# Optimization experiments

Measured on AMD Instinct MI355X. Metric: run time of the kernel, lower is better.

## Reference

```python
import jax, jax.numpy as jnp
import numpy as np

B, M, N, Z = 4, 64, 64, 64
IN_DIM, OUT_DIM = 32, 32
MODES1 = MODES2 = MODES3 = 16
HIDDEN = OUT_DIM * 4  # factor=4, n_ff_layers=2
LN_EPS = 1e-5


def setup_inputs() -> dict:
    key = jax.random.key(0)
    ks = jax.random.split(key, 10)
    # xavier-normal-ish scale for (in, out, modes, 2) fourier weights
    fscale = np.sqrt(2.0 / (IN_DIM + OUT_DIM))
    x = jax.random.normal(ks[0], (B, M, N, Z, IN_DIM), dtype=jnp.float32)
    wx = jax.random.normal(ks[1], (IN_DIM, OUT_DIM, MODES1, 2), dtype=jnp.float32) * fscale
    wy = jax.random.normal(ks[2], (IN_DIM, OUT_DIM, MODES2, 2), dtype=jnp.float32) * fscale
    wz = jax.random.normal(ks[3], (IN_DIM, OUT_DIM, MODES3, 2), dtype=jnp.float32) * fscale
    # FeedForward: Linear(OUT_DIM, HIDDEN) + ReLU, then Linear(HIDDEN, OUT_DIM) + LayerNorm
    w0 = jax.random.normal(ks[4], (OUT_DIM, HIDDEN), dtype=jnp.float32) * np.sqrt(1.0 / OUT_DIM)
    b0 = jnp.zeros((HIDDEN,), dtype=jnp.float32)
    w1 = jax.random.normal(ks[5], (HIDDEN, OUT_DIM), dtype=jnp.float32) * np.sqrt(1.0 / HIDDEN)
    b1 = jnp.zeros((OUT_DIM,), dtype=jnp.float32)
    ln_g = jnp.ones((OUT_DIM,), dtype=jnp.float32)
    ln_b = jnp.zeros((OUT_DIM,), dtype=jnp.float32)
    return {"x": x, "wx": wx, "wy": wy, "wz": wz,
            "w0": w0, "b0": b0, "w1": w1, "b1": b1,
            "ln_g": ln_g, "ln_b": ln_b}


def _as_complex(w):
    return w[..., 0] + 1j * w[..., 1]


def _forward_fourier(x, wx, wy, wz):
    # x: [b, m, n, z, i] -> [b, i, m, n, z]
    xt = jnp.transpose(x, (0, 4, 1, 2, 3))
    # --- axis M (dim 2) ---
    ftx = jnp.fft.rfft(xt, axis=2, norm='ortho')  # [b, i, M//2+1, n, z] complex
    ox = jnp.einsum('bixyz,iox->boxyz', ftx[:, :, :MODES1], _as_complex(wx))
    ox = jnp.pad(ox, ((0, 0), (0, 0), (0, M // 2 + 1 - MODES1), (0, 0), (0, 0)))
    xx = jnp.fft.irfft(ox, n=M, axis=2, norm='ortho')
    # --- axis N (dim 3) ---
    fty = jnp.fft.rfft(xt, axis=3, norm='ortho')
    oy = jnp.einsum('bixyz,ioy->boxyz', fty[:, :, :, :MODES2], _as_complex(wy))
    oy = jnp.pad(oy, ((0, 0), (0, 0), (0, 0), (0, N // 2 + 1 - MODES2), (0, 0)))
    xy = jnp.fft.irfft(oy, n=N, axis=3, norm='ortho')
    # --- axis Z (dim 4) ---
    ftz = jnp.fft.rfft(xt, axis=4, norm='ortho')
    oz = jnp.einsum('bixyz,ioz->boxyz', ftz[:, :, :, :, :MODES3], _as_complex(wz))
    oz = jnp.pad(oz, ((0, 0), (0, 0), (0, 0), (0, 0), (0, Z // 2 + 1 - MODES3)))
    xz = jnp.fft.irfft(oz, n=Z, axis=4, norm='ortho')
    out = xx + xy + xz  # [b, o, m, n, z]
    return jnp.transpose(out, (0, 2, 3, 4, 1))  # [b, m, n, z, o]


def reference(x, wx, wy, wz, w0, b0, w1, b1, ln_g, ln_b):
    s = _forward_fourier(x, wx, wy, wz)
    h = jax.nn.relu(s @ w0 + b0)
    y = h @ w1 + b1
    mu = jnp.mean(y, axis=-1, keepdims=True)
    var = jnp.mean((y - mu) ** 2, axis=-1, keepdims=True)
    y = (y - mu) * jax.lax.rsqrt(var + LN_EPS) * ln_g + ln_b
    return y
```

## Files before the change

### kernel.cpp

```cpp
#include <hip/hip_runtime.h>
#include <math.h>

typedef __attribute__((ext_vector_type(8))) short short8v;
typedef __attribute__((ext_vector_type(4))) float float4v;

constexpr float THETA = 6.28318530717958647692f / 64.0f;

constexpr int S_B = 64 * 64 * 64 * 32;
constexpr int S_M = 64 * 64 * 32;
constexpr int S_N = 64 * 32;
constexpr int S_Z = 32;

__device__ __forceinline__ unsigned short f2bf(float f) {
    unsigned int u = __builtin_bit_cast(unsigned int, f);
    u += 0x7FFFu + ((u >> 16) & 1u);
    return (unsigned short)(u >> 16);
}

constexpr int WS_TF = 98304, WS_TI = 100352, WS_TOTAL = 102400;

__global__ __launch_bounds__(256)
void setup_frags(const float* __restrict__ wx, const float* __restrict__ wy,
                 const float* __restrict__ wz, unsigned short* __restrict__ W)
{
    int f0 = (blockIdx.x * 256 + threadIdx.x) * 4;
#pragma unroll
    for (int u = 0; u < 4; ++u) {
        int f = f0 + u;
        unsigned short v;
        if (f < WS_TF) {
            int ax = f >> 15, rem = f & 32767;
            int k = rem >> 11;
            int rem2 = rem & 2047;
            int wt = rem2 >> 10, rt = (rem2 >> 9) & 1, l = (rem2 >> 3) & 63, e = rem2 & 7;
            int o = 16 * rt + (l & 15), i = 8 * (l >> 4) + e;
            const float* w = (ax == 0) ? wx : ((ax == 1) ? wy : wz);
            v = f2bf(w[((i * 32 + o) * 16 + k) * 2 + wt]);
        } else if (f < WS_TI) {
            int rem = f - WS_TF;
            int jt = rem >> 10, s = (rem >> 9) & 1, l = (rem >> 3) & 63, e = rem & 7;
            int kk = l & 15, m = 32 * s + 8 * (l >> 4) + e;
            int jm = (kk * m) & 63;
            float ang = THETA * (float)jm;
            v = f2bf(jt == 0 ? cosf(ang) : sinf(ang));
        } else {
            int rem = f - WS_TI;
            int mt = rem >> 9, l = (rem >> 3) & 63, e = rem & 7;
            int mp = 16 * mt + (l & 15), r = 8 * (l >> 4) + e;
            int k = r & 15;
            float sk = (k == 0) ? (1.0f / 64.0f) : (2.0f / 64.0f);
            int jm = (k * mp) & 63;
            float ang = THETA * (float)jm;
            v = f2bf(r < 16 ? sk * cosf(ang) : -sk * sinf(ang));
        }
        W[f] = v;
    }
}

__device__ __forceinline__ int ab_byte(int t, int k, int line, int i) {
    return ((((t * 16 + k) * 16 + line) * 64) + i * 2) ^ (((line ^ k) & 7) << 4);
}
__device__ __forceinline__ int p7i(int o, int line, int r) {
    return (o * 16 + line) * 40 + r;
}

template <int AXIS, bool ACCUM>
__global__ __launch_bounds__(256)
void spectral_mfma(const float* __restrict__ x,
                   const unsigned short* __restrict__ wf,
                   const unsigned short* __restrict__ tf,
                   const unsigned short* __restrict__ ti,
                   float* __restrict__ out)
{
    __shared__ __align__(16) unsigned short AB[16384];
    __shared__ __align__(16) unsigned short P7[20480];

    const int t = threadIdx.x, lane = t & 63, wave = t >> 6;
    const int gq = lane >> 4, c = lane & 15;
    constexpr int stride = (AXIS == 0) ? S_M : ((AXIS == 1) ? S_N : S_Z);
    const int l0 = blockIdx.x * 16;

    short8v tfB[2][2];
#pragma unroll
    for (int jt = 0; jt < 2; ++jt)
#pragma unroll
        for (int s = 0; s < 2; ++s)
            tfB[jt][s] = *reinterpret_cast<const short8v*>(tf + ((jt * 2 + s) * 64 + lane) * 8);

    for (int li = 0; li < 4; ++li) {
        const int line = wave * 4 + li;
        const int l = l0 + line;
        const int b = l >> 12, p1 = (l >> 6) & 63, p2 = l & 63;
        long bs;
        if (AXIS == 0)      bs = (long)b * S_B + (long)p1 * S_N + (long)p2 * S_Z;
        else if (AXIS == 1) bs = (long)b * S_B + (long)p1 * S_M + (long)p2 * S_Z;
        else                bs = (long)b * S_B + (long)p1 * S_M + (long)p2 * S_N;

        float4v acc[2][2];
#pragma unroll
        for (int rt = 0; rt < 2; ++rt)
#pragma unroll
            for (int jt = 0; jt < 2; ++jt)
                acc[rt][jt] = float4v{0.f, 0.f, 0.f, 0.f};

#pragma unroll
        for (int rt = 0; rt < 2; ++rt) {
            const float* xp = x + bs + 16 * rt + c;
#pragma unroll
            for (int s = 0; s < 2; ++s) {
                short8v a;
#pragma unroll
                for (int e = 0; e < 8; ++e)
                    a[e] = (short)f2bf(xp[(long)(32 * s + 8 * gq + e) * stride]);
                acc[rt][0] = __builtin_amdgcn_mfma_f32_16x16x32_bf16(a, tfB[0][s], acc[rt][0], 0, 0, 0);
                acc[rt][1] = __builtin_amdgcn_mfma_f32_16x16x32_bf16(a, tfB[1][s], acc[rt][1], 0, 0, 0);
            }
        }
#pragma unroll
        for (int rt = 0; rt < 2; ++rt)
#pragma unroll
            for (int jt = 0; jt < 2; ++jt) {
                unsigned int lo = (unsigned int)f2bf(acc[rt][jt][0]) | ((unsigned int)f2bf(acc[rt][jt][1]) << 16);
                unsigned int hi = (unsigned int)f2bf(acc[rt][jt][2]) | ((unsigned int)f2bf(acc[rt][jt][3]) << 16);
                *reinterpret_cast<uint2*>(reinterpret_cast<char*>(AB) + ab_byte(jt, c, line, 16 * rt + 4 * gq)) =
                    make_uint2(lo, hi);
            }
    }
    __syncthreads();

    {
        const int t2 = wave >> 1, rt = wave & 1;
        for (int k = 0; k < 16; k += 2) {
            float4v acc2[2];
#pragma unroll
            for (int kk = 0; kk < 2; ++kk) {
                const int kc = k + kk;
                short8v aT = *reinterpret_cast<const short8v*>(reinterpret_cast<const char*>(AB) + ab_byte(0, kc, c, 8 * gq));
                short8v bT = *reinterpret_cast<const short8v*>(reinterpret_cast<const char*>(AB) + ab_byte(1, kc, c, 8 * gq));
                const int w1t = t2 ? 1 : 0, w2t = t2 ? 0 : 1;
                short8v w1 = *reinterpret_cast<const short8v*>(wf + (((kc * 2 + w1t) * 2 + rt) * 64 + lane) * 8);
                short8v w2 = *reinterpret_cast<const short8v*>(wf + (((kc * 2 + w2t) * 2 + rt) * 64 + lane) * 8);
                if (t2) {
                    union { short8v s; unsigned int u[4]; } nb;
                    nb.s = bT;
#pragma unroll
                    for (int j = 0; j < 4; ++j) nb.u[j] ^= 0x80008000u;
                    bT = nb.s;
                }
                float4v a2 = float4v{0.f, 0.f, 0.f, 0.f};
                a2 = __builtin_amdgcn_mfma_f32_16x16x32_bf16(w1, aT, a2, 0, 0, 0);
                a2 = __builtin_amdgcn_mfma_f32_16x16x32_bf16(w2, bT, a2, 0, 0, 0);
                acc2[kk] = a2;
            }
#pragma unroll
            for (int r = 0; r < 4; ++r) {
                unsigned int u = (unsigned int)f2bf(acc2[0][r]) | ((unsigned int)f2bf(acc2[1][r]) << 16);
                *reinterpret_cast<unsigned int*>(&P7[p7i(16 * rt + 4 * gq + r, c, 16 * t2 + k)]) = u;
            }
        }
    }
    __syncthreads();

    short8v tiB[4];
#pragma unroll
    for (int mt = 0; mt < 4; ++mt)
        tiB[mt] = *reinterpret_cast<const short8v*>(ti + (mt * 64 + lane) * 8);

    for (int li = 0; li < 4; ++li) {
        const int line = wave * 4 + li;
        const int l = l0 + line;
        const int b = l >> 12, p1 = (l >> 6) & 63, p2 = l & 63;
        long bs;
        if (AXIS == 0)      bs = (long)b * S_B + (long)p1 * S_N + (long)p2 * S_Z;
        else if (AXIS == 1) bs = (long)b * S_B + (long)p1 * S_M + (long)p2 * S_Z;
        else                bs = (long)b * S_B + (long)p1 * S_M + (long)p2 * S_N;

        short8v pA[2];
        pA[0] = *reinterpret_cast<const short8v*>(&P7[p7i(c,      line, 8 * gq)]);
        pA[1] = *reinterpret_cast<const short8v*>(&P7[p7i(16 + c, line, 8 * gq)]);

#pragma unroll
        for (int rt = 0; rt < 2; ++rt)
#pragma unroll
            for (int mt = 0; mt < 4; ++mt) {
                float4v acc = float4v{0.f, 0.f, 0.f, 0.f};
                acc = __builtin_amdgcn_mfma_f32_16x16x32_bf16(pA[rt], tiB[mt], acc, 0, 0, 0);
                float* op = out + bs + (long)(16 * mt + c) * stride + 16 * rt + 4 * gq;
                if (ACCUM) {
                    float4 old = *reinterpret_cast<const float4*>(op);
                    old.x += acc[0]; old.y += acc[1]; old.z += acc[2]; old.w += acc[3];
                    *reinterpret_cast<float4*>(op) = old;
                } else {
                    *reinterpret_cast<float4*>(op) = make_float4(acc[0], acc[1], acc[2], acc[3]);
                }
            }
    }
}

__global__ __launch_bounds__(256)
void ffn_ln_mfma_kernel(float* __restrict__ io,
                        const float* __restrict__ w0, const float* __restrict__ b0,
                        const float* __restrict__ w1, const float* __restrict__ b1,
                        const float* __restrict__ g,  const float* __restrict__ bb)
{
    __shared__ unsigned short smem[28672];

    const int t = threadIdx.x;
    const int lane = t & 63, wave = t >> 6;
    const int gq = lane >> 4, c = lane & 15;

    for (int s = t; s < 512; s += 256) {
        const int n = s >> 6, ln = s & 63, g2 = ln >> 4, c2 = ln & 15;
        const int kb = n >> 1, nn = n & 1;
        short8v v0, v1;
#pragma unroll
        for (int e = 0; e < 8; ++e) {
            v0[e] = (short)f2bf(w0[(8 * g2 + e) * 128 + n * 16 + c2]);
            v1[e] = (short)f2bf(w1[(32 * kb + 8 * g2 + e) * 32 + nn * 16 + c2]);
        }
        *reinterpret_cast<short8v*>(&smem[s * 8])        = v0;
        *reinterpret_cast<short8v*>(&smem[4096 + s * 8]) = v1;
    }
    __syncthreads();

    float b0v[8], b1v[2], gv[2], bv[2];
#pragma unroll
    for (int n = 0; n < 8; ++n) b0v[n] = b0[n * 16 + c];
#pragma unroll
    for (int n = 0; n < 2; ++n) { b1v[n] = b1[n * 16 + c]; gv[n] = g[n * 16 + c]; bv[n] = bb[n * 16 + c]; }

    const int Hbase = 8192 + wave * 5120;

    for (int ti = 0; ti < 4; ++ti) {
        const int tile = (blockIdx.x * 4 + wave) * 4 + ti;
        const long p0 = (long)tile * 64;
        float* pio = io + p0 * 32;

        short8v af[4];
#pragma unroll
        for (int f = 0; f < 4; ++f) {
            const float* sp = pio + (16 * f + c) * 32 + 8 * gq;
            float4 lo = *reinterpret_cast<const float4*>(sp);
            float4 hi = *reinterpret_cast<const float4*>(sp + 4);
            af[f][0] = (short)f2bf(lo.x); af[f][1] = (short)f2bf(lo.y);
            af[f][2] = (short)f2bf(lo.z); af[f][3] = (short)f2bf(lo.w);
            af[f][4] = (short)f2bf(hi.x); af[f][5] = (short)f2bf(hi.y);
            af[f][6] = (short)f2bf(hi.z); af[f][7] = (short)f2bf(hi.w);
        }

        float4v Y[4][2];
#pragma unroll
        for (int f = 0; f < 4; ++f)
#pragma unroll
            for (int n = 0; n < 2; ++n)
                Y[f][n] = float4v{b1v[n], b1v[n], b1v[n], b1v[n]};

#pragma unroll
        for (int kb = 0; kb < 4; ++kb) {
            const int rb = (kb & 1) * 64;
#pragma unroll
            for (int nn = 0; nn < 2; ++nn) {
                const int n = 2 * kb + nn;
                const short8v wv = *reinterpret_cast<const short8v*>(&smem[(n * 64 + lane) * 8]);
#pragma unroll
                for (int f = 0; f < 4; ++f) {
                    float4v hacc = float4v{b0v[n], b0v[n], b0v[n], b0v[n]};
                    hacc = __builtin_amdgcn_mfma_f32_16x16x32_bf16(af[f], wv, hacc, 0, 0, 0);
#pragma unroll
                    for (int r = 0; r < 4; ++r) {
                        const float hv = fmaxf(hacc[r], 0.0f);
                        smem[Hbase + (rb + 16 * f + 4 * gq + r) * 40 + nn * 16 + c] = f2bf(hv);
                    }
                }
            }
            const short8v wva = *reinterpret_cast<const short8v*>(&smem[4096 + ((kb * 2 + 0) * 64 + lane) * 8]);
            const short8v wvb = *reinterpret_cast<const short8v*>(&smem[4096 + ((kb * 2 + 1) * 64 + lane) * 8]);
#pragma unroll
            for (int f = 0; f < 4; ++f) {
                const short8v a2 = *reinterpret_cast<const short8v*>(&smem[Hbase + (rb + 16 * f + c) * 40 + 8 * gq]);
                Y[f][0] = __builtin_amdgcn_mfma_f32_16x16x32_bf16(a2, wva, Y[f][0], 0, 0, 0);
                Y[f][1] = __builtin_amdgcn_mfma_f32_16x16x32_bf16(a2, wvb, Y[f][1], 0, 0, 0);
            }
        }

#pragma unroll
        for (int f = 0; f < 4; ++f) {
            float sm[4], sq[4];
#pragma unroll
            for (int r = 0; r < 4; ++r) {
                const float v0 = Y[f][0][r], v1 = Y[f][1][r];
                sm[r] = v0 + v1;
                sq[r] = v0 * v0 + v1 * v1;
            }
#pragma unroll
            for (int mask = 1; mask <= 8; mask <<= 1) {
#pragma unroll
                for (int r = 0; r < 4; ++r) {
                    sm[r] += __shfl_xor(sm[r], mask);
                    sq[r] += __shfl_xor(sq[r], mask);
                }
            }
#pragma unroll
            for (int r = 0; r < 4; ++r) {
                const float mu = sm[r] * (1.0f / 32.0f);
                const float var = sq[r] * (1.0f / 32.0f) - mu * mu;
                const float rs = rsqrtf(var + 1e-5f);
                float* op = io + (p0 + 16 * f + 4 * gq + r) * 32;
                op[c]      = (Y[f][0][r] - mu) * rs * gv[0] + bv[0];
                op[16 + c] = (Y[f][1][r] - mu) * rs * gv[1] + bv[1];
            }
        }
    }
}

extern "C" void kernel_launch(void* const* d_in, const int* in_sizes, int n_in,
                              void* d_out, int out_size, void* d_ws, size_t ws_size,
                              hipStream_t stream)
{
    const float* x    = (const float*)d_in[0];
    const float* wx   = (const float*)d_in[1];
    const float* wy   = (const float*)d_in[2];
    const float* wz   = (const float*)d_in[3];
    const float* w0   = (const float*)d_in[4];
    const float* b0   = (const float*)d_in[5];
    const float* w1   = (const float*)d_in[6];
    const float* b1   = (const float*)d_in[7];
    const float* ln_g = (const float*)d_in[8];
    const float* ln_b = (const float*)d_in[9];
    float* out = (float*)d_out;

    unsigned short* wsf = (unsigned short*)d_ws;

    setup_frags<<<100, 256, 0, stream>>>(wx, wy, wz, wsf);

    spectral_mfma<0, false><<<1024, 256, 0, stream>>>(x, wsf + 0 * 32768, wsf + WS_TF, wsf + WS_TI, out);
    spectral_mfma<1, true ><<<1024, 256, 0, stream>>>(x, wsf + 1 * 32768, wsf + WS_TF, wsf + WS_TI, out);
    spectral_mfma<2, true ><<<1024, 256, 0, stream>>>(x, wsf + 2 * 32768, wsf + WS_TF, wsf + WS_TI, out);

    ffn_ln_mfma_kernel<<<1024, 256, 0, stream>>>(out, w0, b0, w1, b1, ln_g, ln_b);
}
```

Measured before the change: 273.6 us.

## Fuse Z-axis spectral pass with FFN and LayerNorm, halve lines per block

```diff
diff --git a/kernel.cpp b/kernel.cpp
--- a/kernel.cpp
+++ b/kernel.cpp
@@ -27,6 +27,7 @@
 #pragma unroll
     for (int u = 0; u < 4; ++u) {
         int f = f0 + u;
+        if (f >= WS_TOTAL) continue;
         unsigned short v;
         if (f < WS_TF) {
             int ax = f >> 15, rem = f & 32767;
@@ -57,11 +58,103 @@
     }
 }
 
-__device__ __forceinline__ int ab_byte(int t, int k, int line, int i) {
-    return ((((t * 16 + k) * 16 + line) * 64) + i * 2) ^ (((line ^ k) & 7) << 4);
-}
-__device__ __forceinline__ int p7i(int o, int line, int r) {
-    return (o * 16 + line) * 40 + r;
+constexpr int AB_SHORTS = 8192;
+__device__ __forceinline__ int ab8(int t, int k, int line, int i) {
+    return ((((t * 16 + k) * 8 + line) * 64) + i * 2) ^ (((line ^ k) & 7) << 4);
+}
+constexpr int P_LS = 1288;
+constexpr int P_SHORTS = 8 * P_LS;
+__device__ __forceinline__ int p8(int line, int o, int r) {
+    return line * P_LS + o * 40 + r;
+}
+
+template <int STRIDE>
+__device__ __forceinline__ void stageF(const float* __restrict__ x,
+                                       const long* base2,
+                                       const unsigned short* __restrict__ tf,
+                                       unsigned short* __restrict__ AB,
+                                       int lane, int wave)
+{
+    const int gq = lane >> 4, c = lane & 15;
+    short8v tfB[2][2];
+#pragma unroll
+    for (int jt = 0; jt < 2; ++jt)
+#pragma unroll
+        for (int s = 0; s < 2; ++s)
+            tfB[jt][s] = *reinterpret_cast<const short8v*>(tf + ((jt * 2 + s) * 64 + lane) * 8);
+
+#pragma unroll
+    for (int li = 0; li < 2; ++li) {
+        const int line = wave * 2 + li;
+        float4v acc[2][2];
+#pragma unroll
+        for (int rt = 0; rt < 2; ++rt)
+#pragma unroll
+            for (int jt = 0; jt < 2; ++jt)
+                acc[rt][jt] = float4v{0.f, 0.f, 0.f, 0.f};
+
+#pragma unroll
+        for (int rt = 0; rt < 2; ++rt) {
+            const float* xp = x + base2[li] + 16 * rt + c;
+#pragma unroll
+            for (int s = 0; s < 2; ++s) {
+                short8v a;
+#pragma unroll
+                for (int e = 0; e < 8; ++e)
+                    a[e] = (short)f2bf(xp[(long)(32 * s + 8 * gq + e) * STRIDE]);
+                acc[rt][0] = __builtin_amdgcn_mfma_f32_16x16x32_bf16(a, tfB[0][s], acc[rt][0], 0, 0, 0);
+                acc[rt][1] = __builtin_amdgcn_mfma_f32_16x16x32_bf16(a, tfB[1][s], acc[rt][1], 0, 0, 0);
+            }
+        }
+#pragma unroll
+        for (int rt = 0; rt < 2; ++rt)
+#pragma unroll
+            for (int jt = 0; jt < 2; ++jt) {
+                unsigned int lo = (unsigned int)f2bf(acc[rt][jt][0]) | ((unsigned int)f2bf(acc[rt][jt][1]) << 16);
+                unsigned int hi = (unsigned int)f2bf(acc[rt][jt][2]) | ((unsigned int)f2bf(acc[rt][jt][3]) << 16);
+                *reinterpret_cast<uint2*>(reinterpret_cast<char*>(AB) + ab8(jt, c, line, 16 * rt + 4 * gq)) =
+                    make_uint2(lo, hi);
+            }
+    }
+}
+
+__device__ __forceinline__ void stageMx(const unsigned short* __restrict__ wf,
+                                        const unsigned short* __restrict__ AB,
+                                        unsigned short* __restrict__ P,
+                                        int lane, int wave)
+{
+    const int gq = lane >> 4, c = lane & 15;
+    const int t2 = wave >> 1, rt = wave & 1, lc = c & 7;
+    for (int k = 0; k < 16; k += 2) {
+        float4v acc2[2];
+#pragma unroll
+        for (int kk = 0; kk < 2; ++kk) {
+            const int kc = k + kk;
+            short8v aT = *reinterpret_cast<const short8v*>(reinterpret_cast<const char*>(AB) + ab8(0, kc, lc, 8 * gq));
+            short8v bT = *reinterpret_cast<const short8v*>(reinterpret_cast<const char*>(AB) + ab8(1, kc, lc, 8 * gq));
+            const int w1t = t2 ? 1 : 0, w2t = t2 ? 0 : 1;
+            short8v w1 = *reinterpret_cast<const short8v*>(wf + (((kc * 2 + w1t) * 2 + rt) * 64 + lane) * 8);
+            short8v w2 = *reinterpret_cast<const short8v*>(wf + (((kc * 2 + w2t) * 2 + rt) * 64 + lane) * 8);
+            if (t2) {
+                union { short8v s; unsigned int u[4]; } nb;
+                nb.s = bT;
+#pragma unroll
+                for (int j = 0; j < 4; ++j) nb.u[j] ^= 0x80008000u;
+                bT = nb.s;
+            }
+            float4v a2 = float4v{0.f, 0.f, 0.f, 0.f};
+            a2 = __builtin_amdgcn_mfma_f32_16x16x32_bf16(w1, aT, a2, 0, 0, 0);
+            a2 = __builtin_amdgcn_mfma_f32_16x16x32_bf16(w2, bT, a2, 0, 0, 0);
+            acc2[kk] = a2;
+        }
+        if (c < 8) {
+#pragma unroll
+            for (int r = 0; r < 4; ++r) {
+                unsigned int u = (unsigned int)f2bf(acc2[0][r]) | ((unsigned int)f2bf(acc2[1][r]) << 16);
+                *reinterpret_cast<unsigned int*>(&P[p8(c, 16 * rt + 4 * gq + r, 16 * t2 + k)]) = u;
+            }
+        }
+    }
 }
 
 template <int AXIS, bool ACCUM>
@@ -72,93 +165,27 @@
                    const unsigned short* __restrict__ ti,
                    float* __restrict__ out)
 {
-    __shared__ __align__(16) unsigned short AB[16384];
-    __shared__ __align__(16) unsigned short P7[20480];
+    __shared__ __align__(16) unsigned short AB[AB_SHORTS];
+    __shared__ __align__(16) unsigned short P[P_SHORTS];
 
     const int t = threadIdx.x, lane = t & 63, wave = t >> 6;
     const int gq = lane >> 4, c = lane & 15;
-    constexpr int stride = (AXIS == 0) ? S_M : ((AXIS == 1) ? S_N : S_Z);
-    const int l0 = blockIdx.x * 16;
-
-    short8v tfB[2][2];
-#pragma unroll
-    for (int jt = 0; jt < 2; ++jt)
-#pragma unroll
-        for (int s = 0; s < 2; ++s)
-            tfB[jt][s] = *reinterpret_cast<const short8v*>(tf + ((jt * 2 + s) * 64 + lane) * 8);
-
-    for (int li = 0; li < 4; ++li) {
-        const int line = wave * 4 + li;
-        const int l = l0 + line;
-        const int b = l >> 12, p1 = (l >> 6) & 63, p2 = l & 63;
-        long bs;
-        if (AXIS == 0)      bs = (long)b * S_B + (long)p1 * S_N + (long)p2 * S_Z;
-        else if (AXIS == 1) bs = (long)b * S_B + (long)p1 * S_M + (long)p2 * S_Z;
-        else                bs = (long)b * S_B + (long)p1 * S_M + (long)p2 * S_N;
-
-        float4v acc[2][2];
-#pragma unroll
-        for (int rt = 0; rt < 2; ++rt)
-#pragma unroll
-            for (int jt = 0; jt < 2; ++jt)
-                acc[rt][jt] = float4v{0.f, 0.f, 0.f, 0.f};
-
-#pragma unroll
-        for (int rt = 0; rt < 2; ++rt) {
-            const float* xp = x + bs + 16 * rt + c;
-#pragma unroll
-            for (int s = 0; s < 2; ++s) {
-                short8v a;
-#pragma unroll
-                for (int e = 0; e < 8; ++e)
-                    a[e] = (short)f2bf(xp[(long)(32 * s + 8 * gq + e) * stride]);
-                acc[rt][0] = __builtin_amdgcn_mfma_f32_16x16x32_bf16(a, tfB[0][s], acc[rt][0], 0, 0, 0);
-                acc[rt][1] = __builtin_amdgcn_mfma_f32_16x16x32_bf16(a, tfB[1][s], acc[rt][1], 0, 0, 0);
-            }
-        }
-#pragma unroll
-        for (int rt = 0; rt < 2; ++rt)
-#pragma unroll
-            for (int jt = 0; jt < 2; ++jt) {
-                unsigned int lo = (unsigned int)f2bf(acc[rt][jt][0]) | ((unsigned int)f2bf(acc[rt][jt][1]) << 16);
-                unsigned int hi = (unsigned int)f2bf(acc[rt][jt][2]) | ((unsigned int)f2bf(acc[rt][jt][3]) << 16);
-                *reinterpret_cast<uint2*>(reinterpret_cast<char*>(AB) + ab_byte(jt, c, line, 16 * rt + 4 * gq)) =
-                    make_uint2(lo, hi);
-            }
-    }
-    __syncthreads();
-
-    {
-        const int t2 = wave >> 1, rt = wave & 1;
-        for (int k = 0; k < 16; k += 2) {
-            float4v acc2[2];
-#pragma unroll
-            for (int kk = 0; kk < 2; ++kk) {
-                const int kc = k + kk;
-                short8v aT = *reinterpret_cast<const short8v*>(reinterpret_cast<const char*>(AB) + ab_byte(0, kc, c, 8 * gq));
-                short8v bT = *reinterpret_cast<const short8v*>(reinterpret_cast<const char*>(AB) + ab_byte(1, kc, c, 8 * gq));
-                const int w1t = t2 ? 1 : 0, w2t = t2 ? 0 : 1;
-                short8v w1 = *reinterpret_cast<const short8v*>(wf + (((kc * 2 + w1t) * 2 + rt) * 64 + lane) * 8);
-                short8v w2 = *reinterpret_cast<const short8v*>(wf + (((kc * 2 + w2t) * 2 + rt) * 64 + lane) * 8);
-                if (t2) {
-                    union { short8v s; unsigned int u[4]; } nb;
-                    nb.s = bT;
-#pragma unroll
-                    for (int j = 0; j < 4; ++j) nb.u[j] ^= 0x80008000u;
-                    bT = nb.s;
-                }
-                float4v a2 = float4v{0.f, 0.f, 0.f, 0.f};
-                a2 = __builtin_amdgcn_mfma_f32_16x16x32_bf16(w1, aT, a2, 0, 0, 0);
-                a2 = __builtin_amdgcn_mfma_f32_16x16x32_bf16(w2, bT, a2, 0, 0, 0);
-                acc2[kk] = a2;
-            }
-#pragma unroll
-            for (int r = 0; r < 4; ++r) {
-                unsigned int u = (unsigned int)f2bf(acc2[0][r]) | ((unsigned int)f2bf(acc2[1][r]) << 16);
-                *reinterpret_cast<unsigned int*>(&P7[p7i(16 * rt + 4 * gq + r, c, 16 * t2 + k)]) = u;
-            }
-        }
-    }
+    constexpr int stride = (AXIS == 0) ? S_M : S_N;
+    const int l0 = blockIdx.x * 8;
+
+    long base2[2];
+#pragma unroll
+    for (int li = 0; li < 2; ++li) {
+        int l = l0 + wave * 2 + li;
+        int b = l >> 12, p1 = (l >> 6) & 63, p2 = l & 63;
+        base2[li] = (AXIS == 0)
+            ? (long)b * S_B + (long)p1 * S_N + (long)p2 * S_Z
+            : (long)b * S_B + (long)p1 * S_M + (long)p2 * S_Z;
+    }
+
+    stageF<stride>(x, base2, tf, AB, lane, wave);
+    __syncthreads();
+    stageMx(wf, AB, P, lane, wave);
     __syncthreads();
 
     short8v tiB[4];
@@ -166,26 +193,19 @@
     for (int mt = 0; mt < 4; ++mt)
         tiB[mt] = *reinterpret_cast<const short8v*>(ti + (mt * 64 + lane) * 8);
 
-    for (int li = 0; li < 4; ++li) {
-        const int line = wave * 4 + li;
-        const int l = l0 + line;
-        const int b = l >> 12, p1 = (l >> 6) & 63, p2 = l & 63;
-        long bs;
-        if (AXIS == 0)      bs = (long)b * S_B + (long)p1 * S_N + (long)p2 * S_Z;
-        else if (AXIS == 1) bs = (long)b * S_B + (long)p1 * S_M + (long)p2 * S_Z;
-        else                bs = (long)b * S_B + (long)p1 * S_M + (long)p2 * S_N;
-
+#pragma unroll
+    for (int li = 0; li < 2; ++li) {
+        const int line = wave * 2 + li;
         short8v pA[2];
-        pA[0] = *reinterpret_cast<const short8v*>(&P7[p7i(c,      line, 8 * gq)]);
-        pA[1] = *reinterpret_cast<const short8v*>(&P7[p7i(16 + c, line, 8 * gq)]);
-
+        pA[0] = *reinterpret_cast<const short8v*>(&P[p8(line, c, 8 * gq)]);
+        pA[1] = *reinterpret_cast<const short8v*>(&P[p8(line, 16 + c, 8 * gq)]);
 #pragma unroll
         for (int rt = 0; rt < 2; ++rt)
 #pragma unroll
             for (int mt = 0; mt < 4; ++mt) {
                 float4v acc = float4v{0.f, 0.f, 0.f, 0.f};
                 acc = __builtin_amdgcn_mfma_f32_16x16x32_bf16(pA[rt], tiB[mt], acc, 0, 0, 0);
-                float* op = out + bs + (long)(16 * mt + c) * stride + 16 * rt + 4 * gq;
+                float* op = out + base2[li] + (long)(16 * mt + c) * stride + 16 * rt + 4 * gq;
                 if (ACCUM) {
                     float4 old = *reinterpret_cast<const float4*>(op);
                     old.x += acc[0]; old.y += acc[1]; old.z += acc[2]; old.w += acc[3];
@@ -198,16 +218,40 @@
 }
 
 __global__ __launch_bounds__(256)
-void ffn_ln_mfma_kernel(float* __restrict__ io,
-                        const float* __restrict__ w0, const float* __restrict__ b0,
-                        const float* __restrict__ w1, const float* __restrict__ b1,
-                        const float* __restrict__ g,  const float* __restrict__ bb)
-{
-    __shared__ unsigned short smem[28672];
-
-    const int t = threadIdx.x;
-    const int lane = t & 63, wave = t >> 6;
+void spectral_fused(const float* __restrict__ x,
+                    const unsigned short* __restrict__ wf,
+                    const unsigned short* __restrict__ tf,
+                    const unsigned short* __restrict__ ti,
+                    const float* __restrict__ w0, const float* __restrict__ b0,
+                    const float* __restrict__ w1, const float* __restrict__ b1,
+                    const float* __restrict__ g,  const float* __restrict__ bb,
+                    float* __restrict__ out)
+{
+    __shared__ __align__(16) unsigned short sm[38976];
+    constexpr int OP = 8192, OS = 18496;
+
+    const int t = threadIdx.x, lane = t & 63, wave = t >> 6;
     const int gq = lane >> 4, c = lane & 15;
+    const int l0 = blockIdx.x * 8;
+
+    long base2[2];
+#pragma unroll
+    for (int li = 0; li < 2; ++li) {
+        int l = l0 + wave * 2 + li;
+        int b = l >> 12, p1 = (l >> 6) & 63, p2 = l & 63;
+        base2[li] = (long)b * S_B + (long)p1 * S_M + (long)p2 * S_N;
+    }
+
+    float b0v[8], b1v[2], gv[2], bvv[2];
+#pragma unroll
+    for (int n = 0; n < 8; ++n) b0v[n] = b0[n * 16 + c];
+#pragma unroll
+    for (int n = 0; n < 2; ++n) { b1v[n] = b1[n * 16 + c]; gv[n] = g[n * 16 + c]; bvv[n] = bb[n * 16 + c]; }
+
+    stageF<S_Z>(x, base2, tf, sm, lane, wave);
+    __syncthreads();
+    stageMx(wf, sm, sm + OP, lane, wave);
+    __syncthreads();
 
     for (int s = t; s < 512; s += 256) {
         const int n = s >> 6, ln = s & 63, g2 = ln >> 4, c2 = ln & 15;
@@ -218,35 +262,49 @@
             v0[e] = (short)f2bf(w0[(8 * g2 + e) * 128 + n * 16 + c2]);
             v1[e] = (short)f2bf(w1[(32 * kb + 8 * g2 + e) * 32 + nn * 16 + c2]);
         }
-        *reinterpret_cast<short8v*>(&smem[s * 8])        = v0;
-        *reinterpret_cast<short8v*>(&smem[4096 + s * 8]) = v1;
-    }
-    __syncthreads();
-
-    float b0v[8], b1v[2], gv[2], bv[2];
-#pragma unroll
-    for (int n = 0; n < 8; ++n) b0v[n] = b0[n * 16 + c];
-#pragma unroll
-    for (int n = 0; n < 2; ++n) { b1v[n] = b1[n * 16 + c]; gv[n] = g[n * 16 + c]; bv[n] = bb[n * 16 + c]; }
-
-    const int Hbase = 8192 + wave * 5120;
-
-    for (int ti = 0; ti < 4; ++ti) {
-        const int tile = (blockIdx.x * 4 + wave) * 4 + ti;
-        const long p0 = (long)tile * 64;
-        float* pio = io + p0 * 32;
+        *reinterpret_cast<short8v*>(&sm[s * 8])        = v0;
+        *reinterpret_cast<short8v*>(&sm[4096 + s * 8]) = v1;
+    }
+
+    short8v tiB[4];
+#pragma unroll
+    for (int mt = 0; mt < 4; ++mt)
+        tiB[mt] = *reinterpret_cast<const short8v*>(ti + (mt * 64 + lane) * 8);
+
+#pragma unroll
+    for (int li = 0; li < 2; ++li) {
+        const int line = wave * 2 + li;
+        const long bs = base2[li];
+        short8v pA[2];
+        pA[0] = *reinterpret_cast<const short8v*>(&sm[OP + p8(line, c, 8 * gq)]);
+        pA[1] = *reinterpret_cast<const short8v*>(&sm[OP + p8(line, 16 + c, 8 * gq)]);
+#pragma unroll
+        for (int rt = 0; rt < 2; ++rt)
+#pragma unroll
+            for (int mt = 0; mt < 4; ++mt) {
+                float4v acc = float4v{0.f, 0.f, 0.f, 0.f};
+                acc = __builtin_amdgcn_mfma_f32_16x16x32_bf16(pA[rt], tiB[mt], acc, 0, 0, 0);
+                const float* op = out + bs + (long)(16 * mt + c) * S_Z + 16 * rt + 4 * gq;
+                float4 old = *reinterpret_cast<const float4*>(op);
+                const float v0 = old.x + acc[0], v1 = old.y + acc[1];
+                const float v2 = old.z + acc[2], v3 = old.w + acc[3];
+                const int si = OS + (line * 64 + 16 * mt + c) * 40 + 16 * rt + 4 * gq;
+                *reinterpret_cast<unsigned int*>(&sm[si])     = (unsigned int)f2bf(v0) | ((unsigned int)f2bf(v1) << 16);
+                *reinterpret_cast<unsigned int*>(&sm[si + 2]) = (unsigned int)f2bf(v2) | ((unsigned int)f2bf(v3) << 16);
+            }
+    }
+    __syncthreads();
+
+    const int Hb = OP + wave * 2560;
+#pragma unroll
+    for (int li = 0; li < 2; ++li) {
+        const int line = wave * 2 + li;
+        const long bs = base2[li];
 
         short8v af[4];
 #pragma unroll
-        for (int f = 0; f < 4; ++f) {
-            const float* sp = pio + (16 * f + c) * 32 + 8 * gq;
-            float4 lo = *reinterpret_cast<const float4*>(sp);
-            float4 hi = *reinterpret_cast<const float4*>(sp + 4);
-            af[f][0] = (short)f2bf(lo.x); af[f][1] = (short)f2bf(lo.y);
-            af[f][2] = (short)f2bf(lo.z); af[f][3] = (short)f2bf(lo.w);
-            af[f][4] = (short)f2bf(hi.x); af[f][5] = (short)f2bf(hi.y);
-            af[f][6] = (short)f2bf(hi.z); af[f][7] = (short)f2bf(hi.w);
-        }
+        for (int f = 0; f < 4; ++f)
+            af[f] = *reinterpret_cast<const short8v*>(&sm[OS + (line * 64 + 16 * f + c) * 40 + 8 * gq]);
 
         float4v Y[4][2];
 #pragma unroll
@@ -257,27 +315,24 @@
 
 #pragma unroll
         for (int kb = 0; kb < 4; ++kb) {
-            const int rb = (kb & 1) * 64;
 #pragma unroll
             for (int nn = 0; nn < 2; ++nn) {
                 const int n = 2 * kb + nn;
-                const short8v wv = *reinterpret_cast<const short8v*>(&smem[(n * 64 + lane) * 8]);
+                const short8v wv = *reinterpret_cast<const short8v*>(&sm[(n * 64 + lane) * 8]);
 #pragma unroll
                 for (int f = 0; f < 4; ++f) {
                     float4v hacc = float4v{b0v[n], b0v[n], b0v[n], b0v[n]};
                     hacc = __builtin_amdgcn_mfma_f32_16x16x32_bf16(af[f], wv, hacc, 0, 0, 0);
 #pragma unroll
-                    for (int r = 0; r < 4; ++r) {
-                        const float hv = fmaxf(hacc[r], 0.0f);
-                        smem[Hbase + (rb + 16 * f + 4 * gq + r) * 40 + nn * 16 + c] = f2bf(hv);
-                    }
+                    for (int r = 0; r < 4; ++r)
+                        sm[Hb + (16 * f + 4 * gq + r) * 40 + nn * 16 + c] = f2bf(fmaxf(hacc[r], 0.f));
                 }
             }
-            const short8v wva = *reinterpret_cast<const short8v*>(&smem[4096 + ((kb * 2 + 0) * 64 + lane) * 8]);
-            const short8v wvb = *reinterpret_cast<const short8v*>(&smem[4096 + ((kb * 2 + 1) * 64 + lane) * 8]);
+            const short8v wva = *reinterpret_cast<const short8v*>(&sm[4096 + ((kb * 2 + 0) * 64 + lane) * 8]);
+            const short8v wvb = *reinterpret_cast<const short8v*>(&sm[4096 + ((kb * 2 + 1) * 64 + lane) * 8]);
 #pragma unroll
             for (int f = 0; f < 4; ++f) {
-                const short8v a2 = *reinterpret_cast<const short8v*>(&smem[Hbase + (rb + 16 * f + c) * 40 + 8 * gq]);
+                const short8v a2 = *reinterpret_cast<const short8v*>(&sm[Hb + (16 * f + c) * 40 + 8 * gq]);
                 Y[f][0] = __builtin_amdgcn_mfma_f32_16x16x32_bf16(a2, wva, Y[f][0], 0, 0, 0);
                 Y[f][1] = __builtin_amdgcn_mfma_f32_16x16x32_bf16(a2, wvb, Y[f][1], 0, 0, 0);
             }
@@ -285,29 +340,29 @@
 
 #pragma unroll
         for (int f = 0; f < 4; ++f) {
-            float sm[4], sq[4];
+            float smv[4], sq[4];
 #pragma unroll
             for (int r = 0; r < 4; ++r) {
                 const float v0 = Y[f][0][r], v1 = Y[f][1][r];
-                sm[r] = v0 + v1;
-                sq[r] = v0 * v0 + v1 * v1;
+                smv[r] = v0 + v1;
+                sq[r]  = v0 * v0 + v1 * v1;
             }
 #pragma unroll
             for (int mask = 1; mask <= 8; mask <<= 1) {
 #pragma unroll
                 for (int r = 0; r < 4; ++r) {
-                    sm[r] += __shfl_xor(sm[r], mask);
-                    sq[r] += __shfl_xor(sq[r], mask);
+                    smv[r] += __shfl_xor(smv[r], mask);
+                    sq[r]  += __shfl_xor(sq[r], mask);
                 }
             }
 #pragma unroll
             for (int r = 0; r < 4; ++r) {
-                const float mu = sm[r] * (1.0f / 32.0f);
+                const float mu = smv[r] * (1.0f / 32.0f);
                 const float var = sq[r] * (1.0f / 32.0f) - mu * mu;
                 const float rs = rsqrtf(var + 1e-5f);
-                float* op = io + (p0 + 16 * f + 4 * gq + r) * 32;
-                op[c]      = (Y[f][0][r] - mu) * rs * gv[0] + bv[0];
-                op[16 + c] = (Y[f][1][r] - mu) * rs * gv[1] + bv[1];
+                float* op = out + bs + (long)(16 * f + 4 * gq + r) * 32;
+                op[c]      = (Y[f][0][r] - mu) * rs * gv[0] + bvv[0];
+                op[16 + c] = (Y[f][1][r] - mu) * rs * gv[1] + bvv[1];
             }
         }
     }
@@ -333,9 +388,8 @@
 
     setup_frags<<<100, 256, 0, stream>>>(wx, wy, wz, wsf);
 
-    spectral_mfma<0, false><<<1024, 256, 0, stream>>>(x, wsf + 0 * 32768, wsf + WS_TF, wsf + WS_TI, out);
-    spectral_mfma<1, true ><<<1024, 256, 0, stream>>>(x, wsf + 1 * 32768, wsf + WS_TF, wsf + WS_TI, out);
-    spectral_mfma<2, true ><<<1024, 256, 0, stream>>>(x, wsf + 2 * 32768, wsf + WS_TF, wsf + WS_TI, out);
-
-    ffn_ln_mfma_kernel<<<1024, 256, 0, stream>>>(out, w0, b0, w1, b1, ln_g, ln_b);
-}
+    spectral_mfma<0, false><<<2048, 256, 0, stream>>>(x, wsf + 0 * 32768, wsf + WS_TF, wsf + WS_TI, out);
+    spectral_mfma<1, true ><<<2048, 256, 0, stream>>>(x, wsf + 1 * 32768, wsf + WS_TF, wsf + WS_TI, out);
+    spectral_fused<<<2048, 256, 0, stream>>>(x, wsf + 2 * 32768, wsf + WS_TF, wsf + WS_TI,
+                                             w0, b0, w1, b1, ln_g, ln_b, out);
+}
```

Measured after the change: 260.8 us. 1.05x faster.
